# Optimization experiments

Hardware: AMD Instinct MI355X
Metric: run time of the kernel (lower is better)

Reference implementation:

```python
import jax, jax.numpy as jnp
import numpy as np

WIN = (7, 7)          # window_size (M, M)
DIM = 128             # C
HEADS = 4
B = 64                # images
NW = 64               # windows per image
NG = WIN[0] * WIN[1]  # 49 tokens per window
NT = 3136             # total patches per image (56x56)


def _relative_position_index(wh, ww):
    # Faithful to the TF code (default 'xy' meshgrid ordering, global token at (0,0))
    coords = np.stack(np.meshgrid(np.arange(wh), np.arange(ww)))        # (2, ww, wh)
    flat = coords.reshape(2, wh * ww)                                    # (2, M^2)
    flat1 = np.concatenate([flat, np.array([[0], [0]])], axis=1)         # (2, M^2+1)
    rel = flat[:, :, None] - flat1[:, None, :]                           # (2, M^2, M^2+1)
    rel = rel.transpose(1, 2, 0).astype(np.int32)
    rel[:, :, 0] += wh - 1
    rel[:, :, 1] += ww - 1
    rel[:, :, 0] *= 2 * ww - 1
    return rel.sum(-1)                                                   # (M^2, M^2+1)


def setup_inputs() -> dict:
    key = jax.random.key(0)
    ks = jax.random.split(key, 9)
    C, H = DIM, HEADS
    B_ = B * NW
    table_sz = (2 * WIN[0] - 1) * (2 * WIN[1] - 1)  # 169
    return {
        "x": jax.random.normal(ks[0], (B_, NG, C), jnp.float32),
        "xtotal": jax.random.normal(ks[1], (B, NT, C), jnp.float32),
        "xavg": jax.random.normal(ks[2], (B, 1, C), jnp.float32),
        "mask": jnp.zeros((NW, NG, NG + 1), jnp.float32),
        "W_q": jax.random.normal(ks[3], (C, C), jnp.float32) * (C ** -0.5),
        "b_q": jax.random.normal(ks[4], (C,), jnp.float32) * 0.02,
        "W_kv": jax.random.normal(ks[5], (C, 2 * C), jnp.float32) * (C ** -0.5),
        "b_kv": jax.random.normal(ks[6], (2 * C,), jnp.float32) * 0.02,
        "bias_table": jax.random.normal(ks[7], (table_sz, H), jnp.float32) * 0.02,
        "rel_idx": jnp.asarray(_relative_position_index(*WIN), jnp.int32),
    }


def reference(x, xtotal, xavg, mask, W_q, b_q, W_kv, b_kv, bias_table, rel_idx):
    B_, NGl, C = x.shape
    Bl = xavg.shape[0]
    H = bias_table.shape[1]
    d = C // H
    scale = d ** -0.5
    N = NGl + 1

    # window path: concat repeated global token, project kv / q
    xavgR = jnp.repeat(xavg, B_ // Bl, axis=0)               # (B_, 1, C)
    x_c = jnp.concatenate([x, xavgR], axis=1)                # (B_, N, C)
    kv = (x_c @ W_kv + b_kv).reshape(B_, N, 2, H, d).transpose(2, 0, 3, 1, 4)
    k, v = kv[0], kv[1]                                      # (B_, H, N, d)
    q = ((x @ W_q + b_q).reshape(B_, NGl, H, d).transpose(0, 2, 1, 3)) * scale

    attn = jnp.einsum('bhnd,bhmd->bhnm', q, k)               # (B_, H, NG, N)
    bias = bias_table[rel_idx.reshape(-1)].reshape(NGl, N, H).transpose(2, 0, 1)
    attn = attn + bias[None]
    nW = mask.shape[0]
    attn = attn.reshape(B_ // nW, nW, H, NGl, N) + mask[None, :, None]
    attn = jax.nn.softmax(attn.reshape(B_, H, NGl, N), axis=-1)
    x_out = jnp.einsum('bhnm,bhmd->bhnd', attn, v).transpose(0, 2, 1, 3).reshape(B_, NGl, C)

    # global path: q_avg (NOT scaled in the original), attends over all patches
    Nt = xtotal.shape[1]
    kvg = (xtotal @ W_kv + b_kv).reshape(Bl, Nt, 2, H, d).transpose(2, 0, 3, 1, 4)
    kg, vg = kvg[0], kvg[1]                                  # (B, H, Nt, d)
    q_avg = (xavg @ W_q + b_q).reshape(Bl, 1, H, d).transpose(0, 2, 1, 3)
    attng = jax.nn.softmax(jnp.einsum('bhqd,bhmd->bhqm', q_avg, kg), axis=-1)
    xavg_out = jnp.einsum('bhqm,bhmd->bhqd', attng, vg).transpose(0, 2, 1, 3).reshape(Bl, 1, C)
    return x_out, xavg_out
```

## Files before the change

### kernel.cpp

```cpp
#include <hip/hip_runtime.h>
#include <hip/hip_bf16.h>

#define NB_  4096
#define NG_  49
#define NC_  128
#define NH_  4
#define DH_  32
#define NN_  50
#define NIMG 64
#define NT_  3136
#define SCALE_ 0.17677669529663687f

#define WT_LO_OFF 49152
#define BM_OFF    98304

typedef unsigned short u16;
typedef unsigned int   u32;
typedef __attribute__((ext_vector_type(8))) short bf16x8;
typedef __attribute__((ext_vector_type(4))) float f32x4;

__device__ __forceinline__ float b2f(u16 u) {
    union { u32 i; float f; } v; v.i = ((u32)u) << 16; return v.f;
}
__device__ __forceinline__ u16 f2b(float f) {
    union { float f; u32 i; } v; v.f = f;
    u32 x = v.i;
    return (u16)((x + 0x7fffu + ((x >> 16) & 1u)) >> 16);
}
__device__ __forceinline__ u32 pk2(float a, float b) {
    union { __hip_bfloat162 h2; u32 u; } v;
    v.h2 = __float22bfloat162_rn(make_float2(a, b));
    return v.u;
}

extern "C" __global__ __launch_bounds__(256)
void prep_kernel(const float* __restrict__ Wq, const float* __restrict__ Wkv,
                 const float* __restrict__ btab, const int* __restrict__ ridx,
                 const float* __restrict__ mask, u16* __restrict__ ws)
{
    const int t = threadIdx.x, b = blockIdx.x;
    if (b < 24) {
        const int tn = b, kt = t >> 6, lane = t & 63;
        const int j  = tn * 16 + (lane & 15);
        const int k0 = kt * 32 + (lane >> 4) * 8;
        u32 hi[4], lo[4];
        #pragma unroll
        for (int p = 0; p < 4; ++p) {
            const int k = k0 + 2 * p;
            float w0 = (j < 128) ? Wq[(size_t)k * 128 + j]       : Wkv[(size_t)k * 256 + (j - 128)];
            float w1 = (j < 128) ? Wq[(size_t)(k + 1) * 128 + j] : Wkv[(size_t)(k + 1) * 256 + (j - 128)];
            u16 h0 = f2b(w0), h1 = f2b(w1);
            hi[p] = (u32)h0 | ((u32)h1 << 16);
            lo[p] = (u32)f2b(w0 - b2f(h0)) | ((u32)f2b(w1 - b2f(h1)) << 16);
        }
        const size_t fo = ((size_t)(tn * 4 + kt) * 64 + lane) * 8;
        *(uint4*)(ws + fo)             = make_uint4(hi[0], hi[1], hi[2], hi[3]);
        *(uint4*)(ws + WT_LO_OFF + fo) = make_uint4(lo[0], lo[1], lo[2], lo[3]);
    } else {
        const int idx = (b - 24) * 256 + t;
        const int mq  = idx & 15;
        const int n   = (idx >> 4) & 63;
        const int h   = (idx >> 10) & 3;
        const int wx  = idx >> 12;
        u16 vv[4];
        #pragma unroll
        for (int e = 0; e < 4; ++e) {
            const int m = mq * 4 + e;
            float val = -1e30f;
            if (n < NG_ && m < NN_)
                val = btab[ridx[n * NN_ + m] * NH_ + h] + mask[((size_t)wx * NG_ + n) * NN_ + m];
            vv[e] = f2b(val);
        }
        u32* dst = (u32*)(ws + BM_OFF + ((size_t)((wx * 4 + h) * 64 + n) * 16 + mq) * 4);
        dst[0] = (u32)vv[0] | ((u32)vv[1] << 16);
        dst[1] = (u32)vv[2] | ((u32)vv[3] << 16);
    }
}

struct WinShared {
    u16 xc[64][128];
    u16 q [64][128];
    u16 k [64][128];
    u16 vT[128][64];
};
struct GlobShared {
    float qa[NH_][DH_];
    float xavgS[NC_];
    float u[NH_][NC_];
    float cst[NH_];
    float smax[NH_];
    float ssum[NH_];
    float red[256];
    float wpart[2][NH_][NC_];
    float s[NT_][NH_];
};
union SMem { WinShared w; GlobShared g; };

extern "C" __global__ __launch_bounds__(256, 2)
void wa2_kernel(const float* __restrict__ x, const float* __restrict__ xtotal,
                const float* __restrict__ xavg,
                const float* __restrict__ Wq, const float* __restrict__ bq,
                const float* __restrict__ Wkv, const float* __restrict__ bkv,
                float* __restrict__ out, const u16* __restrict__ ws)
{
    __shared__ SMem sm;
    const int t = threadIdx.x;
    const int blk = blockIdx.x;

    if (blk >= NIMG) {
        WinShared& S = sm.w;
        const int wb   = blk - NIMG;
        const int img  = wb >> 6;
        const int widx = wb & 63;
        const int lane = t & 63, wv = t >> 6;
        const int l15  = lane & 15, g = lane >> 4;

        {
            const float2* xr = (const float2*)(x + (size_t)wb * (NG_ * NC_));
            for (int i = t; i < NG_ * 64; i += 256) {
                const int row = i >> 6, cp = i & 63;
                float2 xv = xr[i];
                *(u32*)&S.xc[row][(2 * cp) ^ ((row & 7) << 3)] = pk2(xv.x, xv.y);
            }
            if (t < 64) {
                float2 av = ((const float2*)(xavg + (size_t)img * NC_))[t];
                *(u32*)&S.xc[49][(2 * t) ^ (1 << 3)] = pk2(av.x, av.y);
            }
            for (int i = t; i < 14 * 64; i += 256) {
                const int row = 50 + (i >> 6), cp = i & 63;
                *(u32*)&S.xc[row][(2 * cp) ^ ((row & 7) << 3)] = 0u;
            }
        }
        __syncthreads();

        {
            const int sw = (l15 & 7) << 3;
            bf16x8 a[4][4];
            #pragma unroll
            for (int tm = 0; tm < 4; ++tm)
                #pragma unroll
                for (int kt = 0; kt < 4; ++kt)
                    a[tm][kt] = *(const bf16x8*)&S.xc[16 * tm + l15][(32 * kt + 8 * g) ^ sw];

            for (int i = 0; i < 6; ++i) {
                const int tn = 6 * wv + i;
                const int jc = tn * 16 + l15;
                f32x4 z = {0.f, 0.f, 0.f, 0.f};
                f32x4 acc[4] = {z, z, z, z};
                #pragma unroll
                for (int kt = 0; kt < 4; ++kt) {
                    const size_t fo = ((size_t)(tn * 4 + kt) * 64 + lane) * 8;
                    bf16x8 bh = *(const bf16x8*)(ws + fo);
                    bf16x8 bl = *(const bf16x8*)(ws + WT_LO_OFF + fo);
                    #pragma unroll
                    for (int tm = 0; tm < 4; ++tm) {
                        acc[tm] = __builtin_amdgcn_mfma_f32_16x16x32_bf16(a[tm][kt], bh, acc[tm], 0, 0, 0);
                        acc[tm] = __builtin_amdgcn_mfma_f32_16x16x32_bf16(a[tm][kt], bl, acc[tm], 0, 0, 0);
                    }
                }
                const float bias = (jc < 128) ? bq[jc] : bkv[jc - 128];
                #pragma unroll
                for (int tm = 0; tm < 4; ++tm) {
                    #pragma unroll
                    for (int r = 0; r < 4; ++r) {
                        const int row = 16 * tm + 4 * g + r;
                        const float vvl = acc[tm][r] + bias;
                        if (jc < 128) {
                            S.q[row][jc ^ ((row & 7) << 3)] = f2b(vvl * SCALE_);
                        } else if (jc < 256) {
                            S.k[row][(jc - 128) ^ ((row & 7) << 3)] = f2b(vvl);
                        } else {
                            const int c = jc - 256;
                            S.vT[c][row ^ ((c & 7) << 3)] = f2b(vvl);
                        }
                    }
                }
            }
        }
        __syncthreads();

        {
            const int h = wv;
            const int sw = (l15 & 7) << 3;
            bf16x8 ka[4], qb[4];
            #pragma unroll
            for (int tk = 0; tk < 4; ++tk)
                ka[tk] = *(const bf16x8*)&S.k[16 * tk + l15][(32 * h + 8 * g) ^ sw];
            #pragma unroll
            for (int tq = 0; tq < 4; ++tq)
                qb[tq] = *(const bf16x8*)&S.q[16 * tq + l15][(32 * h + 8 * g) ^ sw];

            f32x4 s[4][4];
            #pragma unroll
            for (int tk = 0; tk < 4; ++tk)
                #pragma unroll
                for (int tq = 0; tq < 4; ++tq) {
                    f32x4 z = {0.f, 0.f, 0.f, 0.f};
                    s[tk][tq] = __builtin_amdgcn_mfma_f32_16x16x32_bf16(ka[tk], qb[tq], z, 0, 0, 0);
                }

            const u16* bmb = ws + BM_OFF + (size_t)((widx * 4 + h) * 64) * 64;
            #pragma unroll
            for (int tq = 0; tq < 4; ++tq) {
                const int qr = 16 * tq + l15;
                #pragma unroll
                for (int tk = 0; tk < 4; ++tk) {
                    uint2 bm = *(const uint2*)(bmb + qr * 64 + 16 * tk + 4 * g);
                    s[tk][tq][0] += b2f((u16)bm.x);
                    s[tk][tq][1] += b2f((u16)(bm.x >> 16));
                    s[tk][tq][2] += b2f((u16)bm.y);
                    s[tk][tq][3] += b2f((u16)(bm.y >> 16));
                }
            }

            float inv[4];
            #pragma unroll
            for (int tq = 0; tq < 4; ++tq) {
                float m = s[0][tq][0];
                #pragma unroll
                for (int tk = 0; tk < 4; ++tk)
                    #pragma unroll
                    for (int r = 0; r < 4; ++r) m = fmaxf(m, s[tk][tq][r]);
                m = fmaxf(m, __shfl_xor(m, 16));
                m = fmaxf(m, __shfl_xor(m, 32));
                float sum = 0.f;
                #pragma unroll
                for (int tk = 0; tk < 4; ++tk)
                    #pragma unroll
                    for (int r = 0; r < 4; ++r) {
                        float e = __expf(s[tk][tq][r] - m);
                        s[tk][tq][r] = e;
                        sum += e;
                    }
                sum += __shfl_xor(sum, 16);
                sum += __shfl_xor(sum, 32);
                inv[tq] = 1.f / sum;
            }

            bf16x8 pa[4][2];
            #pragma unroll
            for (int tq = 0; tq < 4; ++tq) {
                const float iv = inv[tq];
                #pragma unroll
                for (int kt = 0; kt < 2; ++kt) {
                    union { u32 u[4]; bf16x8 v; } P;
                    P.u[0] = pk2(s[2 * kt][tq][0] * iv, s[2 * kt][tq][1] * iv);
                    P.u[1] = pk2(s[2 * kt][tq][2] * iv, s[2 * kt][tq][3] * iv);
                    P.u[2] = pk2(s[2 * kt + 1][tq][0] * iv, s[2 * kt + 1][tq][1] * iv);
                    P.u[3] = pk2(s[2 * kt + 1][tq][2] * iv, s[2 * kt + 1][tq][3] * iv);
                    pa[tq][kt] = P.v;
                }
            }
            bf16x8 vb[2][2];
            #pragma unroll
            for (int tn = 0; tn < 2; ++tn) {
                const int c = 32 * h + 16 * tn + l15;
                const int swv = (c & 7) << 3;
                #pragma unroll
                for (int kt = 0; kt < 2; ++kt) {
                    union { uint2 u2[2]; bf16x8 v; } B;
                    B.u2[0] = *(const uint2*)&S.vT[c][(32 * kt + 4 * g) ^ swv];
                    B.u2[1] = *(const uint2*)&S.vT[c][(32 * kt + 16 + 4 * g) ^ swv];
                    vb[kt][tn] = B.v;
                }
            }
            #pragma unroll
            for (int tq = 0; tq < 4; ++tq)
                #pragma unroll
                for (int tn = 0; tn < 2; ++tn) {
                    f32x4 acc = {0.f, 0.f, 0.f, 0.f};
                    acc = __builtin_amdgcn_mfma_f32_16x16x32_bf16(pa[tq][0], vb[0][tn], acc, 0, 0, 0);
                    acc = __builtin_amdgcn_mfma_f32_16x16x32_bf16(pa[tq][1], vb[1][tn], acc, 0, 0, 0);
                    #pragma unroll
                    for (int r = 0; r < 4; ++r) {
                        const int row = 16 * tq + 4 * g + r;
                        if (row < NG_)
                            out[(size_t)wb * (NG_ * NC_) + (size_t)row * NC_ + 32 * h + 16 * tn + l15] = acc[r];
                    }
                }
        }
    } else {
        GlobShared& S = sm.g;
        const int img = blk;

        if (t < NC_) S.xavgS[t] = xavg[img * NC_ + t];
        __syncthreads();

        if (t < NC_) {
            const int h = t >> 5, jj = t & 31;
            float acc = bq[h * DH_ + jj];
            for (int c = 0; c < NC_; ++c) acc += S.xavgS[c] * Wq[c * NC_ + h * DH_ + jj];
            S.qa[h][jj] = acc;
        }
        __syncthreads();

        if (t < NC_) {
            const int c = t;
            #pragma unroll
            for (int h = 0; h < NH_; ++h) {
                float acc = 0.f;
                const float* wr = Wkv + (size_t)c * (2 * NC_) + h * DH_;
                #pragma unroll
                for (int jj = 0; jj < DH_; ++jj) acc += wr[jj] * S.qa[h][jj];
                S.u[h][c] = acc;
            }
        } else if (t < NC_ + NH_) {
            const int h = t - NC_;
            float acc = 0.f;
            for (int jj = 0; jj < DH_; ++jj) acc += S.qa[h][jj] * bkv[h * DH_ + jj];
            S.cst[h] = acc;
        }
        __syncthreads();

        float lmax0 = -1e30f, lmax1 = -1e30f, lmax2 = -1e30f, lmax3 = -1e30f;
        for (int m = t; m < NT_; m += 256) {
            const float* xr = xtotal + (size_t)(img * NT_ + m) * NC_;
            float a0 = S.cst[0], a1 = S.cst[1], a2 = S.cst[2], a3 = S.cst[3];
            for (int c = 0; c < NC_; ++c) {
                float xv = xr[c];
                a0 += xv * S.u[0][c];
                a1 += xv * S.u[1][c];
                a2 += xv * S.u[2][c];
                a3 += xv * S.u[3][c];
            }
            S.s[m][0] = a0; S.s[m][1] = a1; S.s[m][2] = a2; S.s[m][3] = a3;
            lmax0 = fmaxf(lmax0, a0); lmax1 = fmaxf(lmax1, a1);
            lmax2 = fmaxf(lmax2, a2); lmax3 = fmaxf(lmax3, a3);
        }
        float lm[NH_] = {lmax0, lmax1, lmax2, lmax3};
        for (int h = 0; h < NH_; ++h) {
            __syncthreads();
            S.red[t] = lm[h];
            __syncthreads();
            for (int off = 128; off > 0; off >>= 1) {
                if (t < off) S.red[t] = fmaxf(S.red[t], S.red[t + off]);
                __syncthreads();
            }
            if (t == 0) S.smax[h] = S.red[0];
        }
        __syncthreads();

        float ls[NH_] = {0.f, 0.f, 0.f, 0.f};
        for (int m = t; m < NT_; m += 256) {
            #pragma unroll
            for (int h = 0; h < NH_; ++h) {
                float e = __expf(S.s[m][h] - S.smax[h]);
                S.s[m][h] = e;
                ls[h] += e;
            }
        }
        for (int h = 0; h < NH_; ++h) {
            __syncthreads();
            S.red[t] = ls[h];
            __syncthreads();
            for (int off = 128; off > 0; off >>= 1) {
                if (t < off) S.red[t] += S.red[t + off];
                __syncthreads();
            }
            if (t == 0) S.ssum[h] = S.red[0];
        }
        __syncthreads();

        {
            const int c = t & 127, half = t >> 7;
            float a0 = 0.f, a1 = 0.f, a2 = 0.f, a3 = 0.f;
            const int m0 = half * (NT_ / 2), m1 = m0 + NT_ / 2;
            for (int m = m0; m < m1; ++m) {
                float xv = xtotal[(size_t)(img * NT_ + m) * NC_ + c];
                a0 += S.s[m][0] * xv; a1 += S.s[m][1] * xv;
                a2 += S.s[m][2] * xv; a3 += S.s[m][3] * xv;
            }
            S.wpart[half][0][c] = a0; S.wpart[half][1][c] = a1;
            S.wpart[half][2][c] = a2; S.wpart[half][3][c] = a3;
        }
        __syncthreads();

        if (t < NC_) {
            const int h = t >> 5;
            const float winv = 1.f / S.ssum[h];
            float acc = bkv[NC_ + t];
            for (int c = 0; c < NC_; ++c) {
                float wv = (S.wpart[0][h][c] + S.wpart[1][h][c]) * winv;
                acc += wv * Wkv[(size_t)c * (2 * NC_) + NC_ + t];
            }
            out[(size_t)NB_ * (NG_ * NC_) + img * NC_ + t] = acc;
        }
    }
}

extern "C" void kernel_launch(void* const* d_in, const int* in_sizes, int n_in,
                              void* d_out, int out_size, void* d_ws, size_t ws_size,
                              hipStream_t stream) {
    const float* x      = (const float*)d_in[0];
    const float* xtotal = (const float*)d_in[1];
    const float* xavg   = (const float*)d_in[2];
    const float* mask   = (const float*)d_in[3];
    const float* Wq     = (const float*)d_in[4];
    const float* bq     = (const float*)d_in[5];
    const float* Wkv    = (const float*)d_in[6];
    const float* bkv    = (const float*)d_in[7];
    const float* btab   = (const float*)d_in[8];
    const int*   ridx   = (const int*)d_in[9];
    float* outp = (float*)d_out;
    u16*   ws   = (u16*)d_ws;
    (void)in_sizes; (void)n_in; (void)out_size; (void)ws_size;

    prep_kernel<<<24 + 1024, 256, 0, stream>>>(Wq, Wkv, btab, ridx, mask, ws);
    wa2_kernel<<<NB_ + NIMG, 256, 0, stream>>>(x, xtotal, xavg, Wq, bq,
                                               Wkv, bkv, outp, (const u16*)ws);
}
```

Measured before the change: 447.7 us.

## Shrink LDS footprint to raise occupancy and fold scale/bias into MFMA setup

The window path now reuses a single buffer for both the xc staging and the transposed V, and the global path's per-patch score array moves from shared memory into global workspace. Together these shrink LDS use so launch bounds can go from 2 to 4 blocks per CU. The query scale is folded into the prepped weights, and bias plus the bias/mask tile are loaded as the MFMA accumulator init in fragment layout, which removes the separate add passes. The prep kernel is restructured to one block per window with ridx/btab cached in LDS. The trade-off is that the global blocks now make extra global-memory round trips for the scores, and an extra barrier is added in the window path.

```diff
diff --git a/kernel.cpp b/kernel.cpp
--- a/kernel.cpp
+++ b/kernel.cpp
@@ -13,6 +13,7 @@
 
 #define WT_LO_OFF 49152
 #define BM_OFF    98304
+#define SBUF_F    573440
 
 typedef unsigned short u16;
 typedef unsigned int   u32;
@@ -38,17 +39,20 @@
                  const float* __restrict__ btab, const int* __restrict__ ridx,
                  const float* __restrict__ mask, u16* __restrict__ ws)
 {
+    __shared__ int   ridxS[NG_ * NN_];
+    __shared__ float btabS[169 * NH_];
     const int t = threadIdx.x, b = blockIdx.x;
     if (b < 24) {
         const int tn = b, kt = t >> 6, lane = t & 63;
         const int j  = tn * 16 + (lane & 15);
         const int k0 = kt * 32 + (lane >> 4) * 8;
+        const float qs = (j < 128) ? SCALE_ : 1.f;
         u32 hi[4], lo[4];
         #pragma unroll
         for (int p = 0; p < 4; ++p) {
             const int k = k0 + 2 * p;
-            float w0 = (j < 128) ? Wq[(size_t)k * 128 + j]       : Wkv[(size_t)k * 256 + (j - 128)];
-            float w1 = (j < 128) ? Wq[(size_t)(k + 1) * 128 + j] : Wkv[(size_t)(k + 1) * 256 + (j - 128)];
+            float w0 = ((j < 128) ? Wq[(size_t)k * 128 + j]       : Wkv[(size_t)k * 256 + (j - 128)]) * qs;
+            float w1 = ((j < 128) ? Wq[(size_t)(k + 1) * 128 + j] : Wkv[(size_t)(k + 1) * 256 + (j - 128)]) * qs;
             u16 h0 = f2b(w0), h1 = f2b(w1);
             hi[p] = (u32)h0 | ((u32)h1 << 16);
             lo[p] = (u32)f2b(w0 - b2f(h0)) | ((u32)f2b(w1 - b2f(h1)) << 16);
@@ -57,31 +61,34 @@
         *(uint4*)(ws + fo)             = make_uint4(hi[0], hi[1], hi[2], hi[3]);
         *(uint4*)(ws + WT_LO_OFF + fo) = make_uint4(lo[0], lo[1], lo[2], lo[3]);
     } else {
-        const int idx = (b - 24) * 256 + t;
-        const int mq  = idx & 15;
-        const int n   = (idx >> 4) & 63;
-        const int h   = (idx >> 10) & 3;
-        const int wx  = idx >> 12;
-        u16 vv[4];
-        #pragma unroll
-        for (int e = 0; e < 4; ++e) {
-            const int m = mq * 4 + e;
-            float val = -1e30f;
-            if (n < NG_ && m < NN_)
-                val = btab[ridx[n * NN_ + m] * NH_ + h] + mask[((size_t)wx * NG_ + n) * NN_ + m];
-            vv[e] = f2b(val);
-        }
-        u32* dst = (u32*)(ws + BM_OFF + ((size_t)((wx * 4 + h) * 64 + n) * 16 + mq) * 4);
-        dst[0] = (u32)vv[0] | ((u32)vv[1] << 16);
-        dst[1] = (u32)vv[2] | ((u32)vv[3] << 16);
+        const int wx = b - 24;
+        for (int i = t; i < NG_ * NN_; i += 256) ridxS[i] = ridx[i];
+        for (int i = t; i < 169 * NH_; i += 256) btabS[i] = btab[i];
+        __syncthreads();
+        for (int i = t; i < NH_ * 16 * 64; i += 256) {
+            const int lane = i & 63, tile = (i >> 6) & 15, h = i >> 10;
+            const int n  = 16 * (tile >> 2) + (lane & 15);
+            const int m0 = 16 * (tile & 3) + 4 * (lane >> 4);
+            u16 vv[4];
+            #pragma unroll
+            for (int e = 0; e < 4; ++e) {
+                const int m = m0 + e;
+                float val = -1e30f;
+                if (n < NG_ && m < NN_)
+                    val = btabS[ridxS[n * NN_ + m] * NH_ + h] + mask[((size_t)wx * NG_ + n) * NN_ + m];
+                vv[e] = f2b(val);
+            }
+            u32* dst = (u32*)(ws + BM_OFF + ((size_t)((wx * NH_ + h) * 16 + tile) * 64 + lane) * 4);
+            dst[0] = (u32)vv[0] | ((u32)vv[1] << 16);
+            dst[1] = (u32)vv[2] | ((u32)vv[3] << 16);
+        }
     }
 }
 
 struct WinShared {
-    u16 xc[64][128];
-    u16 q [64][128];
-    u16 k [64][128];
-    u16 vT[128][64];
+    u16 q[64][128];
+    u16 k[64][128];
+    u16 buf[64 * 128];
 };
 struct GlobShared {
     float qa[NH_][DH_];
@@ -92,16 +99,15 @@
     float ssum[NH_];
     float red[256];
     float wpart[2][NH_][NC_];
-    float s[NT_][NH_];
 };
 union SMem { WinShared w; GlobShared g; };
 
-extern "C" __global__ __launch_bounds__(256, 2)
+extern "C" __global__ __launch_bounds__(256, 4)
 void wa2_kernel(const float* __restrict__ x, const float* __restrict__ xtotal,
                 const float* __restrict__ xavg,
                 const float* __restrict__ Wq, const float* __restrict__ bq,
                 const float* __restrict__ Wkv, const float* __restrict__ bkv,
-                float* __restrict__ out, const u16* __restrict__ ws)
+                float* __restrict__ out, u16* __restrict__ ws)
 {
     __shared__ SMem sm;
     const int t = threadIdx.x;
@@ -116,37 +122,43 @@
         const int l15  = lane & 15, g = lane >> 4;
 
         {
+            u16* xc = S.buf;
             const float2* xr = (const float2*)(x + (size_t)wb * (NG_ * NC_));
             for (int i = t; i < NG_ * 64; i += 256) {
                 const int row = i >> 6, cp = i & 63;
                 float2 xv = xr[i];
-                *(u32*)&S.xc[row][(2 * cp) ^ ((row & 7) << 3)] = pk2(xv.x, xv.y);
+                *(u32*)&xc[row * 128 + ((2 * cp) ^ ((row & 7) << 3))] = pk2(xv.x, xv.y);
             }
             if (t < 64) {
                 float2 av = ((const float2*)(xavg + (size_t)img * NC_))[t];
-                *(u32*)&S.xc[49][(2 * t) ^ (1 << 3)] = pk2(av.x, av.y);
+                *(u32*)&xc[49 * 128 + ((2 * t) ^ 8)] = pk2(av.x, av.y);
             }
             for (int i = t; i < 14 * 64; i += 256) {
                 const int row = 50 + (i >> 6), cp = i & 63;
-                *(u32*)&S.xc[row][(2 * cp) ^ ((row & 7) << 3)] = 0u;
-            }
-        }
+                *(u32*)&xc[row * 128 + ((2 * cp) ^ ((row & 7) << 3))] = 0u;
+            }
+        }
+        __syncthreads();
+
+        const int sw = (l15 & 7) << 3;
+
+        bf16x8 a[4][4];
+        #pragma unroll
+        for (int tm = 0; tm < 4; ++tm)
+            #pragma unroll
+            for (int kt = 0; kt < 4; ++kt)
+                a[tm][kt] = *(const bf16x8*)&S.buf[(16 * tm + l15) * 128 + ((32 * kt + 8 * g) ^ sw)];
         __syncthreads();
 
         {
-            const int sw = (l15 & 7) << 3;
-            bf16x8 a[4][4];
-            #pragma unroll
-            for (int tm = 0; tm < 4; ++tm)
-                #pragma unroll
-                for (int kt = 0; kt < 4; ++kt)
-                    a[tm][kt] = *(const bf16x8*)&S.xc[16 * tm + l15][(32 * kt + 8 * g) ^ sw];
-
+            u16* vT = S.buf;
             for (int i = 0; i < 6; ++i) {
                 const int tn = 6 * wv + i;
                 const int jc = tn * 16 + l15;
-                f32x4 z = {0.f, 0.f, 0.f, 0.f};
-                f32x4 acc[4] = {z, z, z, z};
+                const float bias = (jc < 128) ? bq[jc] * SCALE_ : bkv[jc - 128];
+                f32x4 acc[4];
+                #pragma unroll
+                for (int tm = 0; tm < 4; ++tm) acc[tm] = (f32x4){bias, bias, bias, bias};
                 #pragma unroll
                 for (int kt = 0; kt < 4; ++kt) {
                     const size_t fo = ((size_t)(tn * 4 + kt) * 64 + lane) * 8;
@@ -158,20 +170,23 @@
                         acc[tm] = __builtin_amdgcn_mfma_f32_16x16x32_bf16(a[tm][kt], bl, acc[tm], 0, 0, 0);
                     }
                 }
-                const float bias = (jc < 128) ? bq[jc] : bkv[jc - 128];
                 #pragma unroll
                 for (int tm = 0; tm < 4; ++tm) {
                     #pragma unroll
-                    for (int r = 0; r < 4; ++r) {
-                        const int row = 16 * tm + 4 * g + r;
-                        const float vvl = acc[tm][r] + bias;
+                    for (int rp = 0; rp < 2; ++rp) {
+                        const int r0 = 16 * tm + 4 * g + 2 * rp;
+                        const u32 p = pk2(acc[tm][2 * rp], acc[tm][2 * rp + 1]);
                         if (jc < 128) {
-                            S.q[row][jc ^ ((row & 7) << 3)] = f2b(vvl * SCALE_);
+                            S.q[r0][jc ^ ((r0 & 7) << 3)]           = (u16)p;
+                            S.q[r0 + 1][jc ^ (((r0 + 1) & 7) << 3)] = (u16)(p >> 16);
                         } else if (jc < 256) {
-                            S.k[row][(jc - 128) ^ ((row & 7) << 3)] = f2b(vvl);
+                            const int c = jc - 128;
+                            S.k[r0][c ^ ((r0 & 7) << 3)]           = (u16)p;
+                            S.k[r0 + 1][c ^ (((r0 + 1) & 7) << 3)] = (u16)(p >> 16);
                         } else {
-                            const int c = jc - 256;
-                            S.vT[c][row ^ ((c & 7) << 3)] = f2b(vvl);
+                            const int c = jc - 256, swc = (c & 7) << 3;
+                            vT[c * 64 + (r0 ^ swc)]       = (u16)p;
+                            vT[c * 64 + ((r0 + 1) ^ swc)] = (u16)(p >> 16);
                         }
                     }
                 }
@@ -181,7 +196,7 @@
 
         {
             const int h = wv;
-            const int sw = (l15 & 7) << 3;
+            const u16* vT = S.buf;
             bf16x8 ka[4], qb[4];
             #pragma unroll
             for (int tk = 0; tk < 4; ++tk)
@@ -190,28 +205,18 @@
             for (int tq = 0; tq < 4; ++tq)
                 qb[tq] = *(const bf16x8*)&S.q[16 * tq + l15][(32 * h + 8 * g) ^ sw];
 
+            const u16* bmb = ws + BM_OFF + (size_t)(widx * NH_ + h) * 4096;
             f32x4 s[4][4];
             #pragma unroll
-            for (int tk = 0; tk < 4; ++tk)
-                #pragma unroll
-                for (int tq = 0; tq < 4; ++tq) {
-                    f32x4 z = {0.f, 0.f, 0.f, 0.f};
-                    s[tk][tq] = __builtin_amdgcn_mfma_f32_16x16x32_bf16(ka[tk], qb[tq], z, 0, 0, 0);
-                }
-
-            const u16* bmb = ws + BM_OFF + (size_t)((widx * 4 + h) * 64) * 64;
-            #pragma unroll
-            for (int tq = 0; tq < 4; ++tq) {
-                const int qr = 16 * tq + l15;
+            for (int tq = 0; tq < 4; ++tq)
                 #pragma unroll
                 for (int tk = 0; tk < 4; ++tk) {
-                    uint2 bm = *(const uint2*)(bmb + qr * 64 + 16 * tk + 4 * g);
-                    s[tk][tq][0] += b2f((u16)bm.x);
-                    s[tk][tq][1] += b2f((u16)(bm.x >> 16));
-                    s[tk][tq][2] += b2f((u16)bm.y);
-                    s[tk][tq][3] += b2f((u16)(bm.y >> 16));
-                }
-            }
+                    uint2 bm = *(const uint2*)(bmb + ((size_t)(tq * 4 + tk) * 64 + lane) * 4);
+                    f32x4 c0;
+                    c0[0] = b2f((u16)bm.x); c0[1] = b2f((u16)(bm.x >> 16));
+                    c0[2] = b2f((u16)bm.y); c0[3] = b2f((u16)(bm.y >> 16));
+                    s[tk][tq] = __builtin_amdgcn_mfma_f32_16x16x32_bf16(ka[tk], qb[tq], c0, 0, 0, 0);
+                }
 
             float inv[4];
             #pragma unroll
@@ -259,8 +264,8 @@
                 #pragma unroll
                 for (int kt = 0; kt < 2; ++kt) {
                     union { uint2 u2[2]; bf16x8 v; } B;
-                    B.u2[0] = *(const uint2*)&S.vT[c][(32 * kt + 4 * g) ^ swv];
-                    B.u2[1] = *(const uint2*)&S.vT[c][(32 * kt + 16 + 4 * g) ^ swv];
+                    B.u2[0] = *(const uint2*)&vT[c * 64 + ((32 * kt + 4 * g) ^ swv)];
+                    B.u2[1] = *(const uint2*)&vT[c * 64 + ((32 * kt + 16 + 4 * g) ^ swv)];
                     vb[kt][tn] = B.v;
                 }
             }
@@ -282,6 +287,7 @@
     } else {
         GlobShared& S = sm.g;
         const int img = blk;
+        float* sb = (float*)ws + SBUF_F + (size_t)img * (NT_ * NH_);
 
         if (t < NC_) S.xavgS[t] = xavg[img * NC_ + t];
         __syncthreads();
@@ -323,7 +329,7 @@
                 a2 += xv * S.u[2][c];
                 a3 += xv * S.u[3][c];
             }
-            S.s[m][0] = a0; S.s[m][1] = a1; S.s[m][2] = a2; S.s[m][3] = a3;
+            *(float4*)&sb[m * NH_] = make_float4(a0, a1, a2, a3);
             lmax0 = fmaxf(lmax0, a0); lmax1 = fmaxf(lmax1, a1);
             lmax2 = fmaxf(lmax2, a2); lmax3 = fmaxf(lmax3, a3);
         }
@@ -342,12 +348,12 @@
 
         float ls[NH_] = {0.f, 0.f, 0.f, 0.f};
         for (int m = t; m < NT_; m += 256) {
-            #pragma unroll
-            for (int h = 0; h < NH_; ++h) {
-                float e = __expf(S.s[m][h] - S.smax[h]);
-                S.s[m][h] = e;
-                ls[h] += e;
-            }
+            float4 sv = *(const float4*)&sb[m * NH_];
+            sv.x = __expf(sv.x - S.smax[0]); ls[0] += sv.x;
+            sv.y = __expf(sv.y - S.smax[1]); ls[1] += sv.y;
+            sv.z = __expf(sv.z - S.smax[2]); ls[2] += sv.z;
+            sv.w = __expf(sv.w - S.smax[3]); ls[3] += sv.w;
+            *(float4*)&sb[m * NH_] = sv;
         }
         for (int h = 0; h < NH_; ++h) {
             __syncthreads();
@@ -367,8 +373,9 @@
             const int m0 = half * (NT_ / 2), m1 = m0 + NT_ / 2;
             for (int m = m0; m < m1; ++m) {
                 float xv = xtotal[(size_t)(img * NT_ + m) * NC_ + c];
-                a0 += S.s[m][0] * xv; a1 += S.s[m][1] * xv;
-                a2 += S.s[m][2] * xv; a3 += S.s[m][3] * xv;
+                float4 e4 = *(const float4*)&sb[m * NH_];
+                a0 += e4.x * xv; a1 += e4.y * xv;
+                a2 += e4.z * xv; a3 += e4.w * xv;
             }
             S.wpart[half][0][c] = a0; S.wpart[half][1][c] = a1;
             S.wpart[half][2][c] = a2; S.wpart[half][3][c] = a3;
@@ -405,7 +412,7 @@
     u16*   ws   = (u16*)d_ws;
     (void)in_sizes; (void)n_in; (void)out_size; (void)ws_size;
 
-    prep_kernel<<<24 + 1024, 256, 0, stream>>>(Wq, Wkv, btab, ridx, mask, ws);
+    prep_kernel<<<24 + 64, 256, 0, stream>>>(Wq, Wkv, btab, ridx, mask, ws);
     wa2_kernel<<<NB_ + NIMG, 256, 0, stream>>>(x, xtotal, xavg, Wq, bq,
-                                               Wkv, bkv, outp, (const u16*)ws);
-}
+                                               Wkv, bkv, outp, ws);
+}
```

After: 463.4 us. 1.03x slower.
